# Performance work log

Measured on AMD Instinct MI355X. Metric: run time of the kernel, lower is better.

Reference implementation:

```python
import jax, jax.numpy as jnp
import numpy as np

LAMBDA = 25.0
MU = 25.0
NU = 1.0
ALPHA = 0.25
EPS = 1e-4
NUM_MATCHES = (20, 4)


def _cdist(x, y):
    # x: (B, L1, C), y: (B, L2, C) -> (B, L1, L2) euclidean distances
    x2 = jnp.sum(x * x, axis=-1)[..., :, None]
    y2 = jnp.sum(y * y, axis=-1)[..., None, :]
    d2 = x2 + y2 - 2.0 * jnp.einsum('blc,bmc->blm', x, y)
    return jnp.sqrt(jnp.maximum(d2, 0.0))


def _nearest_neighbors(input_maps, candidate_maps, distances, num_matches):
    # For each input location, its nearest candidate; then keep the
    # num_matches input locations with smallest NN distance, in original order.
    nn_dist = jnp.min(distances, axis=-1)    # (B, L1)
    nn_idx = jnp.argmin(distances, axis=-1)  # (B, L1)
    _, sel = jax.lax.top_k(-nn_dist, num_matches)  # (B, M) smallest distances
    sel = jnp.sort(sel, axis=1)  # restore original ordering of positions
    filtered_input = jnp.take_along_axis(input_maps, sel[..., None], axis=1)
    nn_sel = jnp.take_along_axis(nn_idx, sel, axis=1)
    filtered_candidate = jnp.take_along_axis(candidate_maps, nn_sel[..., None], axis=1)
    return filtered_input, filtered_candidate


def _mse(a, b):
    return jnp.mean((a - b) ** 2)


def _vicreg_loss(z_a, z_b):
    inv_loss = _mse(z_a, z_b)

    def var_loss(z):
        std = jnp.sqrt(jnp.var(z, axis=0, ddof=1) + EPS)
        return jnp.mean(jax.nn.relu(1.0 - std))

    def cov_loss(z):
        n, d = z.shape
        zc = z - jnp.mean(z, axis=0)
        cov = (zc.T @ zc) / (n - 1)
        off = cov - jnp.diag(jnp.diag(cov))
        return jnp.sum(off ** 2) / d

    v = 0.5 * (var_loss(z_a) + var_loss(z_b))
    c = cov_loss(z_a) + cov_loss(z_b)
    return LAMBDA * inv_loss + MU * v + NU * c


def _local_loss(z_global, z_local, grid_global, grid_local):
    B = z_global.shape[0]
    zg = z_global.reshape(B, -1, z_global.shape[-1])   # (B, Lg, C)
    zl = z_local.reshape(B, -1, z_local.shape[-1])     # (B, Ll, C)

    inv_loss = 0.0
    # feature-space NN
    gf, gn = _nearest_neighbors(zg, zl, _cdist(zg, zl), NUM_MATCHES[0])
    lf, ln = _nearest_neighbors(zl, zg, _cdist(zl, zg), NUM_MATCHES[1])
    inv_loss = inv_loss + (_mse(gf, gn) / 2 + _mse(lf, ln) / 2)

    # grid-space NN (distances from grids, gather from feature maps)
    gg = grid_global.reshape(B, -1, 2)
    gl = grid_local.reshape(B, -1, 2)
    gf, gn = _nearest_neighbors(zg, zl, _cdist(gg, gl), NUM_MATCHES[0])
    lf, ln = _nearest_neighbors(zl, zg, _cdist(gl, gg), NUM_MATCHES[1])
    inv_loss = inv_loss + (_mse(gf, gn) / 2 + _mse(lf, ln) / 2)

    return LAMBDA * inv_loss


def setup_inputs() -> dict:
    key = jax.random.key(0)
    ks = jax.random.split(key, 6)
    B, D, C = 32, 8192, 512
    return {
        'z_global': jax.random.normal(ks[0], (B, D), jnp.float32),
        'z_local': jax.random.normal(ks[1], (B, D), jnp.float32),
        'z_global_local_features': jax.random.normal(ks[2], (B, 24, 24, C), jnp.float32),
        'z_local_local_features': jax.random.normal(ks[3], (B, 16, 16, C), jnp.float32),
        'grid_global': jax.random.uniform(ks[4], (B, 24, 24, 2), jnp.float32),
        'grid_local': jax.random.uniform(ks[5], (B, 16, 16, 2), jnp.float32),
    }


def reference(z_global, z_local, z_global_local_features, z_local_local_features, grid_global, grid_local):
    global_loss = _vicreg_loss(z_global, z_local)
    local_loss = _local_loss(z_global_local_features, z_local_local_features, grid_global, grid_local)
    return ALPHA * global_loss + (1.0 - ALPHA) * local_loss
```

## Files before the change

kernel.cpp:

```cpp
#include <hip/hip_runtime.h>
#include <hip/hip_bf16.h>

#define BATCH 32
#define DZ    8192
#define LG    576
#define LL    256
#define CH    512

#define OFF_S      0
#define OFF_BSUM   8192
#define OFF_SELSUM 9472
#define OFF_NG     10496
#define OFF_NL     84224
#define OFF_ROWNN  116992
#define OFF_COLNN  264448
#define OFF_ABF    329984
#define OFF_BBF    19204352
#define WS_NEED    27592960

typedef __attribute__((ext_vector_type(8))) short bf16x8;
typedef __attribute__((ext_vector_type(4))) float f32x4;

__device__ __forceinline__ unsigned short f2bf(float x) {
  union { __hip_bfloat16 h; unsigned short u; } cv;
  cv.h = __float2bfloat16(x);
  return cv.u;
}

__global__ __launch_bounds__(256) void k_front(
    const float* __restrict__ za, const float* __restrict__ zb,
    double* __restrict__ bsum, float* __restrict__ S,
    const float* __restrict__ zgf, const float* __restrict__ zlf,
    unsigned short* __restrict__ Abf, unsigned short* __restrict__ Bbf,
    float* __restrict__ ng, float* __restrict__ nl,
    unsigned long long* __restrict__ nnInit) {
  __shared__ float sred[4][5];
  int tid = threadIdx.x, lane = tid & 63, wv = tid >> 6;
  int blk = blockIdx.x;
  if (blk >= 1088) {
    int row = (blk - 1088) * 4 + wv;
    if (lane == 0) nnInit[row] = ~0ull;
    const float* src; unsigned short* dst; float* nrm;
    if (row < BATCH * LG) {
      src = zgf + (size_t)row * CH; dst = Abf + (size_t)row * CH; nrm = ng + row;
    } else {
      int rr = row - BATCH * LG;
      src = zlf + (size_t)rr * CH; dst = Bbf + (size_t)rr * CH; nrm = nl + rr;
    }
    const float4* s4 = (const float4*)src;
    float4 v0 = s4[lane * 2], v1 = s4[lane * 2 + 1];
    float ss = v0.x * v0.x + v0.y * v0.y + v0.z * v0.z + v0.w * v0.w +
               v1.x * v1.x + v1.y * v1.y + v1.z * v1.z + v1.w * v1.w;
    union { unsigned short h[8]; uint4 u; } pk;
    pk.h[0] = f2bf(v0.x); pk.h[1] = f2bf(v0.y); pk.h[2] = f2bf(v0.z); pk.h[3] = f2bf(v0.w);
    pk.h[4] = f2bf(v1.x); pk.h[5] = f2bf(v1.y); pk.h[6] = f2bf(v1.z); pk.h[7] = f2bf(v1.w);
    *(uint4*)(dst + lane * 8) = pk.u;
    for (int off = 32; off; off >>= 1) ss += __shfl_down(ss, off);
    if (lane == 0) *nrm = ss;
    return;
  }
  if (blk < 32) {
    int i = blk * 256 + tid;
    float sa = 0.f, qa = 0.f, sb = 0.f, qb = 0.f, si = 0.f;
    #pragma unroll 8
    for (int b = 0; b < BATCH; ++b) {
      float va = za[(size_t)b * DZ + i];
      float vb = zb[(size_t)b * DZ + i];
      sa += va; qa += va * va;
      sb += vb; qb += vb * vb;
      float d = va - vb; si += d * d;
    }
    float ssa = qa - sa * sa * (1.f / 32.f);
    float ssb = qb - sb * sb * (1.f / 32.f);
    float v0 = si;
    float v1 = fmaxf(0.f, 1.f - sqrtf(ssa * (1.f / 31.f) + 1e-4f));
    float v2 = fmaxf(0.f, 1.f - sqrtf(ssb * (1.f / 31.f) + 1e-4f));
    float v3 = ssa * ssa, v4 = ssb * ssb;
    for (int off = 32; off; off >>= 1) {
      v0 += __shfl_down(v0, off); v1 += __shfl_down(v1, off);
      v2 += __shfl_down(v2, off); v3 += __shfl_down(v3, off);
      v4 += __shfl_down(v4, off);
    }
    if (lane == 0) {
      sred[wv][0] = v0; sred[wv][1] = v1; sred[wv][2] = v2;
      sred[wv][3] = v3; sred[wv][4] = v4;
    }
    __syncthreads();
    if (tid < 5)
      bsum[blk * 5 + tid] =
          (double)(sred[0][tid] + sred[1][tid] + sred[2][tid] + sred[3][tid]);
  } else {
    int e = blk - 32;
    int zi = e >= 528; if (zi) e -= 528;
    const float* z = zi ? zb : za;
    float* Sz = S + zi * 1024;
    int p = 0, rem = e;
    while (rem >= 32 - p) { rem -= 32 - p; ++p; }
    int q = p + rem;
    const float4* zp = (const float4*)(z + (size_t)p * DZ);
    const float4* zq = (const float4*)(z + (size_t)q * DZ);
    float s = 0.f;
    #pragma unroll
    for (int ii = 0; ii < 8; ++ii) {
      int i = tid + ii * 256;
      float4 a = zp[i], b = zq[i];
      s += a.x * b.x + a.y * b.y + a.z * b.z + a.w * b.w;
    }
    for (int off = 32; off; off >>= 1) s += __shfl_down(s, off);
    if (lane == 0) sred[wv][0] = s;
    __syncthreads();
    if (tid == 0) {
      float r = sred[0][0] + sred[1][0] + sred[2][0] + sred[3][0];
      Sz[p * 32 + q] = r;
      if (p != q) Sz[q * 32 + p] = r;
    }
  }
}

__global__ __launch_bounds__(256) void k_feat_mfma(
    const unsigned short* __restrict__ Abf, const unsigned short* __restrict__ Bbf,
    const float* __restrict__ ng, const float* __restrict__ nl,
    unsigned long long* __restrict__ rowNN, unsigned long long* __restrict__ colNN) {
  const int b = blockIdx.z;
  const int row0 = blockIdx.x * 64;
  const int col0 = blockIdx.y * 128;
  const int tid = threadIdx.x;
  const int wave = tid >> 6, lane = tid & 63;
  const int m16 = lane & 15, quad = lane >> 4;
  const int wm = wave >> 1, wn = wave & 1;

  __shared__ unsigned short As[64][72];
  __shared__ unsigned short Bs[128][72];

  const unsigned short* Ag = Abf + ((size_t)(b * LG + row0)) * CH;
  const unsigned short* Bg = Bbf + ((size_t)(b * LL + col0)) * CH;

  const int sr = tid >> 2, sq = tid & 3;
  const int br = tid >> 1, bq = tid & 1;

  f32x4 acc[2][4] = {};

  for (int k0 = 0; k0 < CH; k0 += 64) {
    uint4 a0 = *(const uint4*)(Ag + (size_t)sr * CH + k0 + sq * 16);
    uint4 a1 = *(const uint4*)(Ag + (size_t)sr * CH + k0 + sq * 16 + 8);
    uint4 b0 = *(const uint4*)(Bg + (size_t)br * CH + k0 + bq * 16);
    uint4 b1 = *(const uint4*)(Bg + (size_t)br * CH + k0 + bq * 16 + 8);
    uint4 b2 = *(const uint4*)(Bg + (size_t)br * CH + k0 + bq * 16 + 32);
    uint4 b3 = *(const uint4*)(Bg + (size_t)br * CH + k0 + bq * 16 + 40);
    __syncthreads();
    *(uint4*)&As[sr][sq * 16] = a0; *(uint4*)&As[sr][sq * 16 + 8] = a1;
    *(uint4*)&Bs[br][bq * 16] = b0; *(uint4*)&Bs[br][bq * 16 + 8] = b1;
    *(uint4*)&Bs[br][bq * 16 + 32] = b2; *(uint4*)&Bs[br][bq * 16 + 40] = b3;
    __syncthreads();
    #pragma unroll
    for (int kk = 0; kk < 64; kk += 32) {
      bf16x8 af0 = *(const bf16x8*)&As[wm * 32 + m16][kk + quad * 8];
      bf16x8 af1 = *(const bf16x8*)&As[wm * 32 + 16 + m16][kk + quad * 8];
      bf16x8 bfv[4];
      #pragma unroll
      for (int j = 0; j < 4; ++j)
        bfv[j] = *(const bf16x8*)&Bs[wn * 64 + j * 16 + m16][kk + quad * 8];
      #pragma unroll
      for (int j = 0; j < 4; ++j) {
        acc[0][j] = __builtin_amdgcn_mfma_f32_16x16x32_bf16(af0, bfv[j], acc[0][j], 0, 0, 0);
        acc[1][j] = __builtin_amdgcn_mfma_f32_16x16x32_bf16(af1, bfv[j], acc[1][j], 0, 0, 0);
      }
    }
  }

  float na[2][4], nb[4];
  #pragma unroll
  for (int i = 0; i < 2; ++i)
    #pragma unroll
    for (int r = 0; r < 4; ++r)
      na[i][r] = ng[b * LG + row0 + wm * 32 + i * 16 + quad * 4 + r];
  #pragma unroll
  for (int j = 0; j < 4; ++j)
    nb[j] = nl[b * LL + col0 + wn * 64 + j * 16 + m16];

  #pragma unroll
  for (int i = 0; i < 2; ++i) {
    #pragma unroll
    for (int r = 0; r < 4; ++r) {
      unsigned long long p = ~0ull;
      #pragma unroll
      for (int j = 0; j < 4; ++j) {
        float d = fmaxf(na[i][r] + nb[j] - 2.f * acc[i][j][r], 0.f);
        unsigned c = (unsigned)(col0 + wn * 64 + j * 16 + m16);
        unsigned long long pj = (((unsigned long long)__float_as_uint(d)) << 32) | c;
        p = pj < p ? pj : p;
      }
      #pragma unroll
      for (int s = 1; s < 16; s <<= 1) {
        unsigned long long q = __shfl_xor(p, s);
        p = q < p ? q : p;
      }
      if (m16 == 0)
        atomicMin(&rowNN[(size_t)b * LG + row0 + wm * 32 + i * 16 + quad * 4 + r], p);
    }
  }
  #pragma unroll
  for (int j = 0; j < 4; ++j) {
    unsigned long long p = ~0ull;
    #pragma unroll
    for (int i = 0; i < 2; ++i) {
      #pragma unroll
      for (int r = 0; r < 4; ++r) {
        float d = fmaxf(na[i][r] + nb[j] - 2.f * acc[i][j][r], 0.f);
        unsigned rg = (unsigned)(row0 + wm * 32 + i * 16 + quad * 4 + r);
        unsigned long long pr = (((unsigned long long)__float_as_uint(d)) << 32) | rg;
        p = pr < p ? pr : p;
      }
    }
    unsigned long long q = __shfl_xor(p, 16); p = q < p ? q : p;
    q = __shfl_xor(p, 32); p = q < p ? q : p;
    if (quad == 0)
      atomicMin(&colNN[(size_t)b * LL + col0 + wn * 64 + j * 16 + m16], p);
  }
}

__global__ __launch_bounds__(64) void k_norms(
    const float* __restrict__ zgf, const float* __restrict__ zlf,
    float* __restrict__ ng, float* __restrict__ nl,
    unsigned long long* __restrict__ nnInit) {
  int r = blockIdx.x;
  if (threadIdx.x == 0) nnInit[r] = ~0ull;
  const float* src; float* dst;
  if (r < BATCH * LG) { src = zgf + (size_t)r * CH; dst = ng + r; }
  else { int rr = r - BATCH * LG; src = zlf + (size_t)rr * CH; dst = nl + rr; }
  float s = 0.f;
  for (int j = threadIdx.x; j < CH; j += 64) { float v = src[j]; s += v * v; }
  for (int off = 32; off > 0; off >>= 1) s += __shfl_down(s, off);
  if (threadIdx.x == 0) *dst = s;
}

__global__ __launch_bounds__(256) void k_feat_nn(
    const float* __restrict__ zgf, const float* __restrict__ zlf,
    const float* __restrict__ ng, const float* __restrict__ nl,
    unsigned long long* __restrict__ rowNN, unsigned long long* __restrict__ colNN) {
  const int b = blockIdx.z;
  const int row0 = blockIdx.x * 64;
  const int col0 = blockIdx.y * 128;
  const int tid = threadIdx.x;
  const int tx = tid & 15, ty = tid >> 4;
  __shared__ float As[64][20];
  __shared__ float Bs[128][20];
  __shared__ float Ds[64][130];
  const float* Ag = zgf + ((size_t)b * LG + row0) * CH;
  const float* Bg = zlf + ((size_t)b * LL + col0) * CH;
  float acc[4][8];
  #pragma unroll
  for (int i = 0; i < 4; ++i)
    #pragma unroll
    for (int j = 0; j < 8; ++j) acc[i][j] = 0.f;
  const int ar = tid >> 2;
  const int ak = (tid & 3) * 4;
  for (int k0 = 0; k0 < CH; k0 += 16) {
    float4 av  = *(const float4*)(Ag + (size_t)ar * CH + k0 + ak);
    float4 bv0 = *(const float4*)(Bg + (size_t)ar * CH + k0 + ak);
    float4 bv1 = *(const float4*)(Bg + (size_t)(ar + 64) * CH + k0 + ak);
    __syncthreads();
    *(float4*)&As[ar][ak] = av;
    *(float4*)&Bs[ar][ak] = bv0;
    *(float4*)&Bs[ar + 64][ak] = bv1;
    __syncthreads();
    #pragma unroll
    for (int k = 0; k < 16; ++k) {
      float a0 = As[ty][k], a1 = As[ty + 16][k], a2 = As[ty + 32][k], a3 = As[ty + 48][k];
      float bv[8];
      #pragma unroll
      for (int j = 0; j < 8; ++j) bv[j] = Bs[tx + 16 * j][k];
      #pragma unroll
      for (int j = 0; j < 8; ++j) {
        acc[0][j] += a0 * bv[j]; acc[1][j] += a1 * bv[j];
        acc[2][j] += a2 * bv[j]; acc[3][j] += a3 * bv[j];
      }
    }
  }
  float ngr[4], nlc[8];
  #pragma unroll
  for (int i = 0; i < 4; ++i) ngr[i] = ng[b * LG + row0 + ty + 16 * i];
  #pragma unroll
  for (int j = 0; j < 8; ++j) nlc[j] = nl[b * LL + col0 + tx + 16 * j];
  #pragma unroll
  for (int i = 0; i < 4; ++i)
    #pragma unroll
    for (int j = 0; j < 8; ++j)
      Ds[ty + 16 * i][tx + 16 * j] = fmaxf(ngr[i] + nlc[j] - 2.f * acc[i][j], 0.f);
  __syncthreads();
  if (tid < 64) {
    unsigned long long best = ~0ull;
    for (int c = 0; c < 128; ++c) {
      unsigned long long p =
          ((unsigned long long)__float_as_uint(Ds[tid][c]) << 32) | (unsigned)(col0 + c);
      best = p < best ? p : best;
    }
    atomicMin(&rowNN[(size_t)b * LG + row0 + tid], best);
  } else if (tid < 192) {
    int c = tid - 64;
    unsigned long long best = ~0ull;
    for (int r = 0; r < 64; ++r) {
      unsigned long long p =
          ((unsigned long long)__float_as_uint(Ds[r][c]) << 32) | (unsigned)(row0 + r);
      best = p < best ? p : best;
    }
    atomicMin(&colNN[(size_t)b * LL + col0 + c], best);
  }
}

struct SelSmem {
  unsigned long long keys[LG];
  unsigned int nnm[LG];
  float cxy[2 * LG];
  unsigned int plist[40];
  unsigned int cnt;
  float fred[4];
};

template <int V>
__device__ __forceinline__ void sel_case(
    SelSmem& sm, int b,
    const float* __restrict__ zgf, const float* __restrict__ zlf,
    const float* __restrict__ gg, const float* __restrict__ gl,
    const unsigned long long* __restrict__ rowNN,
    const unsigned long long* __restrict__ colNN,
    double* __restrict__ selsum) {
  constexpr bool GDIR = (V == 0 || V == 2);
  constexpr int L1 = GDIR ? LG : LL;
  constexpr int L2 = GDIR ? LL : LG;
  constexpr int M  = GDIR ? 20 : 4;
  constexpr int NR = (L1 + 255) / 256;
  const float* fin  = GDIR ? zgf + (size_t)b * LG * CH : zlf + (size_t)b * LL * CH;
  const float* fcan = GDIR ? zlf + (size_t)b * LL * CH : zgf + (size_t)b * LG * CH;
  int tid = threadIdx.x, lane = tid & 63, wv = tid >> 6;
  if (tid == 0) sm.cnt = 0;

  if constexpr (V < 2) {
    const unsigned long long* src =
        (V == 0) ? rowNN + (size_t)b * LG : colNN + (size_t)b * LL;
    #pragma unroll
    for (int s = 0; s < NR; ++s) {
      int l = tid + s * 256;
      if (l < L1) {
        unsigned long long p = src[l];
        sm.keys[l] = (p & 0xFFFFFFFF00000000ull) | (unsigned)l;
        sm.nnm[l] = (unsigned)(p & 0xFFFFFFFFu);
      }
    }
  } else {
    const float* gin  = (V == 2) ? gg + (size_t)b * LG * 2 : gl + (size_t)b * LL * 2;
    const float* gcan = (V == 2) ? gl + (size_t)b * LL * 2 : gg + (size_t)b * LG * 2;
    #pragma unroll
    for (int s = 0; s < (2 * L2 + 255) / 256; ++s) {
      int i = tid + s * 256;
      if (i < 2 * L2) sm.cxy[i] = gcan[i];
    }
    __syncthreads();
    float x[NR], y[NR], bd[NR];
    unsigned bi[NR];
    #pragma unroll
    for (int s = 0; s < NR; ++s) {
      int l = tid + s * 256;
      x[s] = (l < L1) ? gin[2 * l] : 0.f;
      y[s] = (l < L1) ? gin[2 * l + 1] : 0.f;
      bd[s] = 3.4e38f; bi[s] = 0;
    }
    const float2* c2 = (const float2*)sm.cxy;
    for (int m2 = 0; m2 < L2; m2 += 8) {
      float2 cc[8];
      #pragma unroll
      for (int u = 0; u < 8; ++u) cc[u] = c2[m2 + u];
      #pragma unroll
      for (int u = 0; u < 8; ++u)
        #pragma unroll
        for (int s = 0; s < NR; ++s) {
          float dx = x[s] - cc[u].x, dy = y[s] - cc[u].y;
          float d2 = dx * dx + dy * dy;
          if (d2 < bd[s]) { bd[s] = d2; bi[s] = (unsigned)(m2 + u); }
        }
    }
    #pragma unroll
    for (int s = 0; s < NR; ++s) {
      int l = tid + s * 256;
      if (l < L1) {
        sm.keys[l] = ((unsigned long long)__float_as_uint(bd[s]) << 32) | (unsigned)l;
        sm.nnm[l] = bi[s];
      }
    }
  }
  __syncthreads();

  unsigned long long myk[NR];
  int rk[NR];
  #pragma unroll
  for (int s = 0; s < NR; ++s) {
    int l = tid + s * 256;
    myk[s] = (l < L1) ? sm.keys[l] : ~0ull;
    rk[s] = 0;
  }
  for (int j = 0; j < L1; j += 8) {
    unsigned long long kk[8];
    #pragma unroll
    for (int u = 0; u < 8; ++u) kk[u] = sm.keys[j + u];
    #pragma unroll
    for (int u = 0; u < 8; ++u)
      #pragma unroll
      for (int s = 0; s < NR; ++s) rk[s] += (kk[u] < myk[s]) ? 1 : 0;
  }
  #pragma unroll
  for (int s = 0; s < NR; ++s) {
    int l = tid + s * 256;
    if (l < L1 && rk[s] < M) {
      unsigned slot = atomicAdd(&sm.cnt, 1u);
      sm.plist[2 * slot] = (unsigned)l;
      sm.plist[2 * slot + 1] = sm.nnm[l];
    }
  }
  __syncthreads();

  float part = 0.f;
  #pragma unroll
  for (int rr = 0; rr < M / 4; ++rr) {
    int r = wv + rr * 4;
    const float4* a4 = (const float4*)(fin + (size_t)sm.plist[2 * r] * CH);
    const float4* c4 = (const float4*)(fcan + (size_t)sm.plist[2 * r + 1] * CH);
    float4 xa = a4[lane * 2], xb = a4[lane * 2 + 1];
    float4 ya = c4[lane * 2], yb = c4[lane * 2 + 1];
    float d0 = xa.x - ya.x, d1 = xa.y - ya.y, d2 = xa.z - ya.z, d3 = xa.w - ya.w;
    float d4 = xb.x - yb.x, d5 = xb.y - yb.y, d6 = xb.z - yb.z, d7 = xb.w - yb.w;
    part += d0 * d0 + d1 * d1 + d2 * d2 + d3 * d3 +
            d4 * d4 + d5 * d5 + d6 * d6 + d7 * d7;
  }
  for (int s = 32; s; s >>= 1) part += __shfl_down(part, s);
  if (lane == 0) sm.fred[wv] = part;
  __syncthreads();
  if (tid == 0)
    selsum[V * 32 + b] = (double)(sm.fred[0] + sm.fred[1] + sm.fred[2] + sm.fred[3]);
}

__global__ __launch_bounds__(256) void k_sel(
    const float* __restrict__ zgf, const float* __restrict__ zlf,
    const float* __restrict__ gg, const float* __restrict__ gl,
    const unsigned long long* __restrict__ rowNN,
    const unsigned long long* __restrict__ colNN,
    double* __restrict__ selsum) {
  __shared__ SelSmem sm;
  int b = blockIdx.x;
  switch (blockIdx.y) {
    case 0: sel_case<0>(sm, b, zgf, zlf, gg, gl, rowNN, colNN, selsum); break;
    case 1: sel_case<1>(sm, b, zgf, zlf, gg, gl, rowNN, colNN, selsum); break;
    case 2: sel_case<2>(sm, b, zgf, zlf, gg, gl, rowNN, colNN, selsum); break;
    default: sel_case<3>(sm, b, zgf, zlf, gg, gl, rowNN, colNN, selsum); break;
  }
}

__global__ __launch_bounds__(64) void k_final(
    const double* __restrict__ bsum, const double* __restrict__ selsum,
    const float* __restrict__ S, float* __restrict__ out) {
  __shared__ float t[2][32];
  __shared__ double sacc[5];
  __shared__ double smf[4];
  int lane = threadIdx.x;
  #pragma unroll
  for (int zi = 0; zi < 2; ++zi) {
    if (lane < 32) {
      float tp = 0.f;
      for (int bb = 0; bb < 32; ++bb) tp += S[zi * 1024 + lane * 32 + bb];
      t[zi][lane] = tp * (1.f / 32.f);
    }
  }
  if (lane < 5) {
    double s = 0.0;
    for (int blk = 0; blk < 32; ++blk) s += bsum[blk * 5 + lane];
    sacc[lane] = s;
  }
  if (lane >= 8 && lane < 12) {
    int v = lane - 8;
    double s = 0.0;
    for (int bb = 0; bb < 32; ++bb) s += selsum[v * 32 + bb];
    smf[v] = s;
  }
  __syncthreads();
  double total[2];
  #pragma unroll
  for (int zi = 0; zi < 2; ++zi) {
    float u = 0.f;
    for (int bb = 0; bb < 32; ++bb) u += t[zi][bb];
    u *= (1.f / 32.f);
    double s = 0.0;
    for (int e = lane; e < 1024; e += 64) {
      int p = e >> 5, q = e & 31;
      float G = S[zi * 1024 + e] - t[zi][p] - t[zi][q] + u;
      s += (double)G * (double)G;
    }
    for (int off = 32; off; off >>= 1) s += __shfl_down(s, off);
    total[zi] = s;
  }
  if (lane == 0) {
    double inv_g = sacc[0] / (32.0 * 8192.0);
    double v = 0.5 * (sacc[1] + sacc[2]) / 8192.0;
    double c = (total[0] - sacc[3] + total[1] - sacc[4]) / (961.0 * 8192.0);
    double gloss = 25.0 * inv_g + 25.0 * v + c;
    double mfg = smf[0] / (32.0 * 20.0 * 512.0);
    double mfl = smf[1] / (32.0 * 4.0 * 512.0);
    double mgg = smf[2] / (32.0 * 20.0 * 512.0);
    double mgl = smf[3] / (32.0 * 4.0 * 512.0);
    double lloss = 25.0 * (0.5 * (mfg + mfl) + 0.5 * (mgg + mgl));
    out[0] = (float)(0.25 * gloss + 0.75 * lloss);
  }
}

extern "C" void kernel_launch(void* const* d_in, const int* in_sizes, int n_in,
                              void* d_out, int out_size, void* d_ws, size_t ws_size,
                              hipStream_t stream) {
  const float* zg  = (const float*)d_in[0];
  const float* zl  = (const float*)d_in[1];
  const float* zgf = (const float*)d_in[2];
  const float* zlf = (const float*)d_in[3];
  const float* gg  = (const float*)d_in[4];
  const float* glo = (const float*)d_in[5];

  char* ws = (char*)d_ws;
  float* S       = (float*)(ws + OFF_S);
  double* bsum   = (double*)(ws + OFF_BSUM);
  double* selsum = (double*)(ws + OFF_SELSUM);
  float* ng = (float*)(ws + OFF_NG);
  float* nl = (float*)(ws + OFF_NL);
  unsigned long long* rowNN = (unsigned long long*)(ws + OFF_ROWNN);
  unsigned long long* colNN = (unsigned long long*)(ws + OFF_COLNN);
  unsigned short* Abf = (unsigned short*)(ws + OFF_ABF);
  unsigned short* Bbf = (unsigned short*)(ws + OFF_BBF);

  if (ws_size >= WS_NEED) {
    k_front<<<32 + 1056 + (BATCH * (LG + LL)) / 4, 256, 0, stream>>>(
        zg, zl, bsum, S, zgf, zlf, Abf, Bbf, ng, nl, rowNN);
    k_feat_mfma<<<dim3(LG / 64, LL / 128, BATCH), 256, 0, stream>>>(
        Abf, Bbf, ng, nl, rowNN, colNN);
  } else {
    k_front<<<32 + 1056, 256, 0, stream>>>(
        zg, zl, bsum, S, zgf, zlf, Abf, Bbf, ng, nl, rowNN);
    k_norms<<<BATCH * (LG + LL), 64, 0, stream>>>(zgf, zlf, ng, nl, rowNN);
    k_feat_nn<<<dim3(LG / 64, LL / 128, BATCH), 256, 0, stream>>>(zgf, zlf, ng, nl, rowNN, colNN);
  }
  k_sel<<<dim3(BATCH, 4), 256, 0, stream>>>(zgf, zlf, gg, glo, rowNN, colNN, selsum);
  k_final<<<1, 64, 0, stream>>>(bsum, selsum, S, (float*)d_out);
}
```

Before: 162.0 us.

## Fuse bf16 conversion and norms into MFMA kernel; merge launches into mega and tail kernels

The features are now converted fp32→bf16 inside the MFMA tile loader, and squared norms are accumulated during the same loads. This removes the separate bf16 workspace pass and its extra global round trip. Nearest-neighbour results are written as per-tile partials and reduced at selection time, which replaces atomicMin and the init pass. The global VICReg work and the grid-space selection cases run in the same launch as the distance GEMM. The final reduction moves into the last tail block via a done counter, cutting launches from four to two. In exchange, the fp32 tiles are reloaded and converted redundantly across column tiles, and tail selection has to read more partial entries.

```diff
diff --git a/kernel.cpp b/kernel.cpp
--- a/kernel.cpp
+++ b/kernel.cpp
@@ -10,13 +10,10 @@
 #define OFF_S      0
 #define OFF_BSUM   8192
 #define OFF_SELSUM 9472
-#define OFF_NG     10496
-#define OFF_NL     84224
-#define OFF_ROWNN  116992
-#define OFF_COLNN  264448
-#define OFF_ABF    329984
-#define OFF_BBF    19204352
-#define WS_NEED    27592960
+#define OFF_DONE   10496
+#define OFF_RNP    10560
+#define OFF_CNP    305472
+#define WS_NEED    895296
 
 typedef __attribute__((ext_vector_type(8))) short bf16x8;
 typedef __attribute__((ext_vector_type(4))) float f32x4;
@@ -27,285 +24,15 @@
   return cv.u;
 }
 
-__global__ __launch_bounds__(256) void k_front(
-    const float* __restrict__ za, const float* __restrict__ zb,
-    double* __restrict__ bsum, float* __restrict__ S,
-    const float* __restrict__ zgf, const float* __restrict__ zlf,
-    unsigned short* __restrict__ Abf, unsigned short* __restrict__ Bbf,
-    float* __restrict__ ng, float* __restrict__ nl,
-    unsigned long long* __restrict__ nnInit) {
-  __shared__ float sred[4][5];
-  int tid = threadIdx.x, lane = tid & 63, wv = tid >> 6;
-  int blk = blockIdx.x;
-  if (blk >= 1088) {
-    int row = (blk - 1088) * 4 + wv;
-    if (lane == 0) nnInit[row] = ~0ull;
-    const float* src; unsigned short* dst; float* nrm;
-    if (row < BATCH * LG) {
-      src = zgf + (size_t)row * CH; dst = Abf + (size_t)row * CH; nrm = ng + row;
-    } else {
-      int rr = row - BATCH * LG;
-      src = zlf + (size_t)rr * CH; dst = Bbf + (size_t)rr * CH; nrm = nl + rr;
-    }
-    const float4* s4 = (const float4*)src;
-    float4 v0 = s4[lane * 2], v1 = s4[lane * 2 + 1];
-    float ss = v0.x * v0.x + v0.y * v0.y + v0.z * v0.z + v0.w * v0.w +
-               v1.x * v1.x + v1.y * v1.y + v1.z * v1.z + v1.w * v1.w;
-    union { unsigned short h[8]; uint4 u; } pk;
-    pk.h[0] = f2bf(v0.x); pk.h[1] = f2bf(v0.y); pk.h[2] = f2bf(v0.z); pk.h[3] = f2bf(v0.w);
-    pk.h[4] = f2bf(v1.x); pk.h[5] = f2bf(v1.y); pk.h[6] = f2bf(v1.z); pk.h[7] = f2bf(v1.w);
-    *(uint4*)(dst + lane * 8) = pk.u;
-    for (int off = 32; off; off >>= 1) ss += __shfl_down(ss, off);
-    if (lane == 0) *nrm = ss;
-    return;
-  }
-  if (blk < 32) {
-    int i = blk * 256 + tid;
-    float sa = 0.f, qa = 0.f, sb = 0.f, qb = 0.f, si = 0.f;
-    #pragma unroll 8
-    for (int b = 0; b < BATCH; ++b) {
-      float va = za[(size_t)b * DZ + i];
-      float vb = zb[(size_t)b * DZ + i];
-      sa += va; qa += va * va;
-      sb += vb; qb += vb * vb;
-      float d = va - vb; si += d * d;
-    }
-    float ssa = qa - sa * sa * (1.f / 32.f);
-    float ssb = qb - sb * sb * (1.f / 32.f);
-    float v0 = si;
-    float v1 = fmaxf(0.f, 1.f - sqrtf(ssa * (1.f / 31.f) + 1e-4f));
-    float v2 = fmaxf(0.f, 1.f - sqrtf(ssb * (1.f / 31.f) + 1e-4f));
-    float v3 = ssa * ssa, v4 = ssb * ssb;
-    for (int off = 32; off; off >>= 1) {
-      v0 += __shfl_down(v0, off); v1 += __shfl_down(v1, off);
-      v2 += __shfl_down(v2, off); v3 += __shfl_down(v3, off);
-      v4 += __shfl_down(v4, off);
-    }
-    if (lane == 0) {
-      sred[wv][0] = v0; sred[wv][1] = v1; sred[wv][2] = v2;
-      sred[wv][3] = v3; sred[wv][4] = v4;
-    }
-    __syncthreads();
-    if (tid < 5)
-      bsum[blk * 5 + tid] =
-          (double)(sred[0][tid] + sred[1][tid] + sred[2][tid] + sred[3][tid]);
-  } else {
-    int e = blk - 32;
-    int zi = e >= 528; if (zi) e -= 528;
-    const float* z = zi ? zb : za;
-    float* Sz = S + zi * 1024;
-    int p = 0, rem = e;
-    while (rem >= 32 - p) { rem -= 32 - p; ++p; }
-    int q = p + rem;
-    const float4* zp = (const float4*)(z + (size_t)p * DZ);
-    const float4* zq = (const float4*)(z + (size_t)q * DZ);
-    float s = 0.f;
-    #pragma unroll
-    for (int ii = 0; ii < 8; ++ii) {
-      int i = tid + ii * 256;
-      float4 a = zp[i], b = zq[i];
-      s += a.x * b.x + a.y * b.y + a.z * b.z + a.w * b.w;
-    }
-    for (int off = 32; off; off >>= 1) s += __shfl_down(s, off);
-    if (lane == 0) sred[wv][0] = s;
-    __syncthreads();
-    if (tid == 0) {
-      float r = sred[0][0] + sred[1][0] + sred[2][0] + sred[3][0];
-      Sz[p * 32 + q] = r;
-      if (p != q) Sz[q * 32 + p] = r;
-    }
-  }
-}
-
-__global__ __launch_bounds__(256) void k_feat_mfma(
-    const unsigned short* __restrict__ Abf, const unsigned short* __restrict__ Bbf,
-    const float* __restrict__ ng, const float* __restrict__ nl,
-    unsigned long long* __restrict__ rowNN, unsigned long long* __restrict__ colNN) {
-  const int b = blockIdx.z;
-  const int row0 = blockIdx.x * 64;
-  const int col0 = blockIdx.y * 128;
-  const int tid = threadIdx.x;
-  const int wave = tid >> 6, lane = tid & 63;
-  const int m16 = lane & 15, quad = lane >> 4;
-  const int wm = wave >> 1, wn = wave & 1;
-
-  __shared__ unsigned short As[64][72];
-  __shared__ unsigned short Bs[128][72];
-
-  const unsigned short* Ag = Abf + ((size_t)(b * LG + row0)) * CH;
-  const unsigned short* Bg = Bbf + ((size_t)(b * LL + col0)) * CH;
-
-  const int sr = tid >> 2, sq = tid & 3;
-  const int br = tid >> 1, bq = tid & 1;
-
-  f32x4 acc[2][4] = {};
-
-  for (int k0 = 0; k0 < CH; k0 += 64) {
-    uint4 a0 = *(const uint4*)(Ag + (size_t)sr * CH + k0 + sq * 16);
-    uint4 a1 = *(const uint4*)(Ag + (size_t)sr * CH + k0 + sq * 16 + 8);
-    uint4 b0 = *(const uint4*)(Bg + (size_t)br * CH + k0 + bq * 16);
-    uint4 b1 = *(const uint4*)(Bg + (size_t)br * CH + k0 + bq * 16 + 8);
-    uint4 b2 = *(const uint4*)(Bg + (size_t)br * CH + k0 + bq * 16 + 32);
-    uint4 b3 = *(const uint4*)(Bg + (size_t)br * CH + k0 + bq * 16 + 40);
-    __syncthreads();
-    *(uint4*)&As[sr][sq * 16] = a0; *(uint4*)&As[sr][sq * 16 + 8] = a1;
-    *(uint4*)&Bs[br][bq * 16] = b0; *(uint4*)&Bs[br][bq * 16 + 8] = b1;
-    *(uint4*)&Bs[br][bq * 16 + 32] = b2; *(uint4*)&Bs[br][bq * 16 + 40] = b3;
-    __syncthreads();
-    #pragma unroll
-    for (int kk = 0; kk < 64; kk += 32) {
-      bf16x8 af0 = *(const bf16x8*)&As[wm * 32 + m16][kk + quad * 8];
-      bf16x8 af1 = *(const bf16x8*)&As[wm * 32 + 16 + m16][kk + quad * 8];
-      bf16x8 bfv[4];
-      #pragma unroll
-      for (int j = 0; j < 4; ++j)
-        bfv[j] = *(const bf16x8*)&Bs[wn * 64 + j * 16 + m16][kk + quad * 8];
-      #pragma unroll
-      for (int j = 0; j < 4; ++j) {
-        acc[0][j] = __builtin_amdgcn_mfma_f32_16x16x32_bf16(af0, bfv[j], acc[0][j], 0, 0, 0);
-        acc[1][j] = __builtin_amdgcn_mfma_f32_16x16x32_bf16(af1, bfv[j], acc[1][j], 0, 0, 0);
-      }
-    }
-  }
-
-  float na[2][4], nb[4];
-  #pragma unroll
-  for (int i = 0; i < 2; ++i)
-    #pragma unroll
-    for (int r = 0; r < 4; ++r)
-      na[i][r] = ng[b * LG + row0 + wm * 32 + i * 16 + quad * 4 + r];
-  #pragma unroll
-  for (int j = 0; j < 4; ++j)
-    nb[j] = nl[b * LL + col0 + wn * 64 + j * 16 + m16];
-
-  #pragma unroll
-  for (int i = 0; i < 2; ++i) {
-    #pragma unroll
-    for (int r = 0; r < 4; ++r) {
-      unsigned long long p = ~0ull;
-      #pragma unroll
-      for (int j = 0; j < 4; ++j) {
-        float d = fmaxf(na[i][r] + nb[j] - 2.f * acc[i][j][r], 0.f);
-        unsigned c = (unsigned)(col0 + wn * 64 + j * 16 + m16);
-        unsigned long long pj = (((unsigned long long)__float_as_uint(d)) << 32) | c;
-        p = pj < p ? pj : p;
-      }
-      #pragma unroll
-      for (int s = 1; s < 16; s <<= 1) {
-        unsigned long long q = __shfl_xor(p, s);
-        p = q < p ? q : p;
-      }
-      if (m16 == 0)
-        atomicMin(&rowNN[(size_t)b * LG + row0 + wm * 32 + i * 16 + quad * 4 + r], p);
-    }
-  }
-  #pragma unroll
-  for (int j = 0; j < 4; ++j) {
-    unsigned long long p = ~0ull;
-    #pragma unroll
-    for (int i = 0; i < 2; ++i) {
-      #pragma unroll
-      for (int r = 0; r < 4; ++r) {
-        float d = fmaxf(na[i][r] + nb[j] - 2.f * acc[i][j][r], 0.f);
-        unsigned rg = (unsigned)(row0 + wm * 32 + i * 16 + quad * 4 + r);
-        unsigned long long pr = (((unsigned long long)__float_as_uint(d)) << 32) | rg;
-        p = pr < p ? pr : p;
-      }
-    }
-    unsigned long long q = __shfl_xor(p, 16); p = q < p ? q : p;
-    q = __shfl_xor(p, 32); p = q < p ? q : p;
-    if (quad == 0)
-      atomicMin(&colNN[(size_t)b * LL + col0 + wn * 64 + j * 16 + m16], p);
-  }
-}
-
-__global__ __launch_bounds__(64) void k_norms(
-    const float* __restrict__ zgf, const float* __restrict__ zlf,
-    float* __restrict__ ng, float* __restrict__ nl,
-    unsigned long long* __restrict__ nnInit) {
-  int r = blockIdx.x;
-  if (threadIdx.x == 0) nnInit[r] = ~0ull;
-  const float* src; float* dst;
-  if (r < BATCH * LG) { src = zgf + (size_t)r * CH; dst = ng + r; }
-  else { int rr = r - BATCH * LG; src = zlf + (size_t)rr * CH; dst = nl + rr; }
-  float s = 0.f;
-  for (int j = threadIdx.x; j < CH; j += 64) { float v = src[j]; s += v * v; }
-  for (int off = 32; off > 0; off >>= 1) s += __shfl_down(s, off);
-  if (threadIdx.x == 0) *dst = s;
-}
-
-__global__ __launch_bounds__(256) void k_feat_nn(
-    const float* __restrict__ zgf, const float* __restrict__ zlf,
-    const float* __restrict__ ng, const float* __restrict__ nl,
-    unsigned long long* __restrict__ rowNN, unsigned long long* __restrict__ colNN) {
-  const int b = blockIdx.z;
-  const int row0 = blockIdx.x * 64;
-  const int col0 = blockIdx.y * 128;
-  const int tid = threadIdx.x;
-  const int tx = tid & 15, ty = tid >> 4;
-  __shared__ float As[64][20];
-  __shared__ float Bs[128][20];
-  __shared__ float Ds[64][130];
-  const float* Ag = zgf + ((size_t)b * LG + row0) * CH;
-  const float* Bg = zlf + ((size_t)b * LL + col0) * CH;
-  float acc[4][8];
-  #pragma unroll
-  for (int i = 0; i < 4; ++i)
-    #pragma unroll
-    for (int j = 0; j < 8; ++j) acc[i][j] = 0.f;
-  const int ar = tid >> 2;
-  const int ak = (tid & 3) * 4;
-  for (int k0 = 0; k0 < CH; k0 += 16) {
-    float4 av  = *(const float4*)(Ag + (size_t)ar * CH + k0 + ak);
-    float4 bv0 = *(const float4*)(Bg + (size_t)ar * CH + k0 + ak);
-    float4 bv1 = *(const float4*)(Bg + (size_t)(ar + 64) * CH + k0 + ak);
-    __syncthreads();
-    *(float4*)&As[ar][ak] = av;
-    *(float4*)&Bs[ar][ak] = bv0;
-    *(float4*)&Bs[ar + 64][ak] = bv1;
-    __syncthreads();
-    #pragma unroll
-    for (int k = 0; k < 16; ++k) {
-      float a0 = As[ty][k], a1 = As[ty + 16][k], a2 = As[ty + 32][k], a3 = As[ty + 48][k];
-      float bv[8];
-      #pragma unroll
-      for (int j = 0; j < 8; ++j) bv[j] = Bs[tx + 16 * j][k];
-      #pragma unroll
-      for (int j = 0; j < 8; ++j) {
-        acc[0][j] += a0 * bv[j]; acc[1][j] += a1 * bv[j];
-        acc[2][j] += a2 * bv[j]; acc[3][j] += a3 * bv[j];
-      }
-    }
-  }
-  float ngr[4], nlc[8];
-  #pragma unroll
-  for (int i = 0; i < 4; ++i) ngr[i] = ng[b * LG + row0 + ty + 16 * i];
-  #pragma unroll
-  for (int j = 0; j < 8; ++j) nlc[j] = nl[b * LL + col0 + tx + 16 * j];
-  #pragma unroll
-  for (int i = 0; i < 4; ++i)
-    #pragma unroll
-    for (int j = 0; j < 8; ++j)
-      Ds[ty + 16 * i][tx + 16 * j] = fmaxf(ngr[i] + nlc[j] - 2.f * acc[i][j], 0.f);
-  __syncthreads();
-  if (tid < 64) {
-    unsigned long long best = ~0ull;
-    for (int c = 0; c < 128; ++c) {
-      unsigned long long p =
-          ((unsigned long long)__float_as_uint(Ds[tid][c]) << 32) | (unsigned)(col0 + c);
-      best = p < best ? p : best;
-    }
-    atomicMin(&rowNN[(size_t)b * LG + row0 + tid], best);
-  } else if (tid < 192) {
-    int c = tid - 64;
-    unsigned long long best = ~0ull;
-    for (int r = 0; r < 64; ++r) {
-      unsigned long long p =
-          ((unsigned long long)__float_as_uint(Ds[r][c]) << 32) | (unsigned)(row0 + r);
-      best = p < best ? p : best;
-    }
-    atomicMin(&colNN[(size_t)b * LL + col0 + c], best);
-  }
+__device__ __forceinline__ uint4 pack8(float4 lo, float4 hi) {
+  union { unsigned short h[8]; uint4 u; } pk;
+  pk.h[0] = f2bf(lo.x); pk.h[1] = f2bf(lo.y); pk.h[2] = f2bf(lo.z); pk.h[3] = f2bf(lo.w);
+  pk.h[4] = f2bf(hi.x); pk.h[5] = f2bf(hi.y); pk.h[6] = f2bf(hi.z); pk.h[7] = f2bf(hi.w);
+  return pk.u;
+}
+
+__device__ __forceinline__ float dot4(float4 v) {
+  return v.x * v.x + v.y * v.y + v.z * v.z + v.w * v.w;
 }
 
 struct SelSmem {
@@ -322,8 +49,8 @@
     SelSmem& sm, int b,
     const float* __restrict__ zgf, const float* __restrict__ zlf,
     const float* __restrict__ gg, const float* __restrict__ gl,
-    const unsigned long long* __restrict__ rowNN,
-    const unsigned long long* __restrict__ colNN,
+    const unsigned long long* __restrict__ rowNNp,
+    const unsigned long long* __restrict__ colNNp,
     double* __restrict__ selsum) {
   constexpr bool GDIR = (V == 0 || V == 2);
   constexpr int L1 = GDIR ? LG : LL;
@@ -336,13 +63,17 @@
   if (tid == 0) sm.cnt = 0;
 
   if constexpr (V < 2) {
+    constexpr int P = (V == 0) ? 2 : 9;
     const unsigned long long* src =
-        (V == 0) ? rowNN + (size_t)b * LG : colNN + (size_t)b * LL;
+        (V == 0) ? rowNNp + (size_t)b * LG * 2 : colNNp + (size_t)b * LL * 9;
     #pragma unroll
     for (int s = 0; s < NR; ++s) {
       int l = tid + s * 256;
       if (l < L1) {
-        unsigned long long p = src[l];
+        const unsigned long long* q = src + (size_t)l * P;
+        unsigned long long p = q[0];
+        #pragma unroll
+        for (int u = 1; u < P; ++u) { unsigned long long t2 = q[u]; p = t2 < p ? t2 : p; }
         sm.keys[l] = (p & 0xFFFFFFFF00000000ull) | (unsigned)l;
         sm.nnm[l] = (unsigned)(p & 0xFFFFFFFFu);
       }
@@ -438,75 +169,291 @@
     selsum[V * 32 + b] = (double)(sm.fred[0] + sm.fred[1] + sm.fred[2] + sm.fred[3]);
 }
 
-__global__ __launch_bounds__(256) void k_sel(
+__global__ __launch_bounds__(256) void k_mega(
+    const float* __restrict__ za, const float* __restrict__ zb,
     const float* __restrict__ zgf, const float* __restrict__ zlf,
     const float* __restrict__ gg, const float* __restrict__ gl,
-    const unsigned long long* __restrict__ rowNN,
-    const unsigned long long* __restrict__ colNN,
-    double* __restrict__ selsum) {
-  __shared__ SelSmem sm;
-  int b = blockIdx.x;
-  switch (blockIdx.y) {
-    case 0: sel_case<0>(sm, b, zgf, zlf, gg, gl, rowNN, colNN, selsum); break;
-    case 1: sel_case<1>(sm, b, zgf, zlf, gg, gl, rowNN, colNN, selsum); break;
-    case 2: sel_case<2>(sm, b, zgf, zlf, gg, gl, rowNN, colNN, selsum); break;
-    default: sel_case<3>(sm, b, zgf, zlf, gg, gl, rowNN, colNN, selsum); break;
-  }
-}
-
-__global__ __launch_bounds__(64) void k_final(
-    const double* __restrict__ bsum, const double* __restrict__ selsum,
-    const float* __restrict__ S, float* __restrict__ out) {
-  __shared__ float t[2][32];
-  __shared__ double sacc[5];
-  __shared__ double smf[4];
-  int lane = threadIdx.x;
-  #pragma unroll
-  for (int zi = 0; zi < 2; ++zi) {
-    if (lane < 32) {
+    double* __restrict__ bsum, float* __restrict__ S,
+    unsigned long long* __restrict__ rowNNp, unsigned long long* __restrict__ colNNp,
+    double* __restrict__ selsum, unsigned int* __restrict__ doneCnt) {
+  __shared__ __align__(16) char smem[28416];
+  int tid = threadIdx.x, lane = tid & 63, wv = tid >> 6;
+  int blk = blockIdx.x;
+
+  if (blk < 576) {
+    int fs = (blk & 7) * 72 + (blk >> 3);
+    int b = fs / 18, rr_ = fs % 18;
+    int by = rr_ / 9, bx = rr_ % 9;
+    int row0 = bx * 64, col0 = by * 128;
+
+    unsigned short (*As)[72] = (unsigned short(*)[72])smem;
+    unsigned short (*Bs)[72] = (unsigned short(*)[72])(smem + 9216);
+    float* Asn = (float*)(smem + 27648);
+    float* Bsn = (float*)(smem + 27904);
+
+    const int m16 = lane & 15, quad = lane >> 4;
+    const int wm = wv >> 1, wn = wv & 1;
+    const float* Ag = zgf + ((size_t)(b * LG + row0)) * CH;
+    const float* Bg = zlf + ((size_t)(b * LL + col0)) * CH;
+    const int sr = tid >> 2, sq = tid & 3;
+    const int br = tid >> 1, bq = tid & 1;
+
+    f32x4 acc[2][4] = {};
+    float ssA = 0.f, ssB = 0.f;
+
+    for (int k0 = 0; k0 < CH; k0 += 64) {
+      const float* ap = Ag + (size_t)sr * CH + k0 + sq * 16;
+      float4 a0 = *(const float4*)(ap);
+      float4 a1 = *(const float4*)(ap + 4);
+      float4 a2 = *(const float4*)(ap + 8);
+      float4 a3 = *(const float4*)(ap + 12);
+      const float* bp = Bg + (size_t)br * CH + k0 + bq * 16;
+      float4 b0 = *(const float4*)(bp);
+      float4 b1 = *(const float4*)(bp + 4);
+      float4 b2 = *(const float4*)(bp + 8);
+      float4 b3 = *(const float4*)(bp + 12);
+      float4 b4 = *(const float4*)(bp + 32);
+      float4 b5 = *(const float4*)(bp + 36);
+      float4 b6 = *(const float4*)(bp + 40);
+      float4 b7 = *(const float4*)(bp + 44);
+      ssA += dot4(a0) + dot4(a1) + dot4(a2) + dot4(a3);
+      ssB += dot4(b0) + dot4(b1) + dot4(b2) + dot4(b3) +
+             dot4(b4) + dot4(b5) + dot4(b6) + dot4(b7);
+      __syncthreads();
+      *(uint4*)&As[sr][sq * 16]      = pack8(a0, a1);
+      *(uint4*)&As[sr][sq * 16 + 8]  = pack8(a2, a3);
+      *(uint4*)&Bs[br][bq * 16]      = pack8(b0, b1);
+      *(uint4*)&Bs[br][bq * 16 + 8]  = pack8(b2, b3);
+      *(uint4*)&Bs[br][bq * 16 + 32] = pack8(b4, b5);
+      *(uint4*)&Bs[br][bq * 16 + 40] = pack8(b6, b7);
+      __syncthreads();
+      #pragma unroll
+      for (int kk = 0; kk < 64; kk += 32) {
+        bf16x8 af0 = *(const bf16x8*)&As[wm * 32 + m16][kk + quad * 8];
+        bf16x8 af1 = *(const bf16x8*)&As[wm * 32 + 16 + m16][kk + quad * 8];
+        bf16x8 bfv[4];
+        #pragma unroll
+        for (int j = 0; j < 4; ++j)
+          bfv[j] = *(const bf16x8*)&Bs[wn * 64 + j * 16 + m16][kk + quad * 8];
+        #pragma unroll
+        for (int j = 0; j < 4; ++j) {
+          acc[0][j] = __builtin_amdgcn_mfma_f32_16x16x32_bf16(af0, bfv[j], acc[0][j], 0, 0, 0);
+          acc[1][j] = __builtin_amdgcn_mfma_f32_16x16x32_bf16(af1, bfv[j], acc[1][j], 0, 0, 0);
+        }
+      }
+    }
+
+    ssA += __shfl_xor(ssA, 1); ssA += __shfl_xor(ssA, 2);
+    ssB += __shfl_xor(ssB, 1);
+    if (sq == 0) Asn[sr] = ssA;
+    if (bq == 0) Bsn[br] = ssB;
+    __syncthreads();
+
+    float na[2][4], nb[4];
+    #pragma unroll
+    for (int i = 0; i < 2; ++i)
+      #pragma unroll
+      for (int r = 0; r < 4; ++r)
+        na[i][r] = Asn[wm * 32 + i * 16 + quad * 4 + r];
+    #pragma unroll
+    for (int j = 0; j < 4; ++j)
+      nb[j] = Bsn[wn * 64 + j * 16 + m16];
+
+    #pragma unroll
+    for (int i = 0; i < 2; ++i) {
+      #pragma unroll
+      for (int r = 0; r < 4; ++r) {
+        unsigned long long p = ~0ull;
+        #pragma unroll
+        for (int j = 0; j < 4; ++j) {
+          float d = fmaxf(na[i][r] + nb[j] - 2.f * acc[i][j][r], 0.f);
+          unsigned c = (unsigned)(col0 + wn * 64 + j * 16 + m16);
+          unsigned long long pj = (((unsigned long long)__float_as_uint(d)) << 32) | c;
+          p = pj < p ? pj : p;
+        }
+        #pragma unroll
+        for (int s = 1; s < 16; s <<= 1) {
+          unsigned long long q = __shfl_xor(p, s);
+          p = q < p ? q : p;
+        }
+        if (m16 == 0)
+          rowNNp[((size_t)b * LG + row0 + wm * 32 + i * 16 + quad * 4 + r) * 2 + by] = p;
+      }
+    }
+    #pragma unroll
+    for (int j = 0; j < 4; ++j) {
+      unsigned long long p = ~0ull;
+      #pragma unroll
+      for (int i = 0; i < 2; ++i) {
+        #pragma unroll
+        for (int r = 0; r < 4; ++r) {
+          float d = fmaxf(na[i][r] + nb[j] - 2.f * acc[i][j][r], 0.f);
+          unsigned rg = (unsigned)(row0 + wm * 32 + i * 16 + quad * 4 + r);
+          unsigned long long pr = (((unsigned long long)__float_as_uint(d)) << 32) | rg;
+          p = pr < p ? pr : p;
+        }
+      }
+      unsigned long long q = __shfl_xor(p, 16); p = q < p ? q : p;
+      q = __shfl_xor(p, 32); p = q < p ? q : p;
+      if (quad == 0)
+        colNNp[((size_t)b * LL + col0 + wn * 64 + j * 16 + m16) * 9 + bx] = p;
+    }
+    return;
+  }
+
+  if (blk < 608) {
+    float (*sred)[5] = (float(*)[5])smem;
+    int blkS = blk - 576;
+    if (blkS == 0 && tid == 0) *doneCnt = 0;
+    int i = blkS * 256 + tid;
+    float sa = 0.f, qa = 0.f, sb = 0.f, qb = 0.f, si = 0.f;
+    #pragma unroll 8
+    for (int b = 0; b < BATCH; ++b) {
+      float va = za[(size_t)b * DZ + i];
+      float vb = zb[(size_t)b * DZ + i];
+      sa += va; qa += va * va;
+      sb += vb; qb += vb * vb;
+      float d = va - vb; si += d * d;
+    }
+    float ssa = qa - sa * sa * (1.f / 32.f);
+    float ssb = qb - sb * sb * (1.f / 32.f);
+    float v0 = si;
+    float v1 = fmaxf(0.f, 1.f - sqrtf(ssa * (1.f / 31.f) + 1e-4f));
+    float v2 = fmaxf(0.f, 1.f - sqrtf(ssb * (1.f / 31.f) + 1e-4f));
+    float v3 = ssa * ssa, v4 = ssb * ssb;
+    for (int off = 32; off; off >>= 1) {
+      v0 += __shfl_down(v0, off); v1 += __shfl_down(v1, off);
+      v2 += __shfl_down(v2, off); v3 += __shfl_down(v3, off);
+      v4 += __shfl_down(v4, off);
+    }
+    if (lane == 0) {
+      sred[wv][0] = v0; sred[wv][1] = v1; sred[wv][2] = v2;
+      sred[wv][3] = v3; sred[wv][4] = v4;
+    }
+    __syncthreads();
+    if (tid < 5)
+      bsum[blkS * 5 + tid] =
+          (double)(sred[0][tid] + sred[1][tid] + sred[2][tid] + sred[3][tid]);
+    return;
+  }
+
+  if (blk < 1664) {
+    float (*sred)[5] = (float(*)[5])smem;
+    int e = blk - 608;
+    int zi = e >= 528; if (zi) e -= 528;
+    const float* z = zi ? zb : za;
+    float* Sz = S + zi * 1024;
+    int p = 0, rem = e;
+    while (rem >= 32 - p) { rem -= 32 - p; ++p; }
+    int q = p + rem;
+    const float4* zp = (const float4*)(z + (size_t)p * DZ);
+    const float4* zq = (const float4*)(z + (size_t)q * DZ);
+    float s = 0.f;
+    #pragma unroll
+    for (int ii = 0; ii < 8; ++ii) {
+      int i = tid + ii * 256;
+      float4 a = zp[i], bb = zq[i];
+      s += a.x * bb.x + a.y * bb.y + a.z * bb.z + a.w * bb.w;
+    }
+    for (int off = 32; off; off >>= 1) s += __shfl_down(s, off);
+    if (lane == 0) sred[wv][0] = s;
+    __syncthreads();
+    if (tid == 0) {
+      float r = sred[0][0] + sred[1][0] + sred[2][0] + sred[3][0];
+      Sz[p * 32 + q] = r;
+      if (p != q) Sz[q * 32 + p] = r;
+    }
+    return;
+  }
+
+  {
+    SelSmem& sm = *reinterpret_cast<SelSmem*>(smem);
+    int e = blk - 1664;
+    int b2 = e >> 1;
+    if (e & 1) sel_case<3>(sm, b2, zgf, zlf, gg, gl, rowNNp, colNNp, selsum);
+    else       sel_case<2>(sm, b2, zgf, zlf, gg, gl, rowNNp, colNNp, selsum);
+  }
+}
+
+struct TailSmem {
+  SelSmem sel;
+  float t[2][32];
+  double sacc[5];
+  double smf[4];
+  int isLast;
+};
+
+__global__ __launch_bounds__(256) void k_tail(
+    const float* __restrict__ zgf, const float* __restrict__ zlf,
+    const float* __restrict__ gg, const float* __restrict__ gl,
+    const unsigned long long* __restrict__ rowNNp,
+    const unsigned long long* __restrict__ colNNp,
+    double* __restrict__ selsum, const double* __restrict__ bsum,
+    const float* __restrict__ S, unsigned int* __restrict__ doneCnt,
+    float* __restrict__ out) {
+  __shared__ TailSmem ts;
+  int tid = threadIdx.x;
+  int b = blockIdx.x >> 1, V = blockIdx.x & 1;
+  if (V == 0) sel_case<0>(ts.sel, b, zgf, zlf, gg, gl, rowNNp, colNNp, selsum);
+  else        sel_case<1>(ts.sel, b, zgf, zlf, gg, gl, rowNNp, colNNp, selsum);
+
+  if (tid == 0) {
+    __threadfence();
+    unsigned r = atomicAdd(doneCnt, 1u);
+    ts.isLast = (r == 63) ? 1 : 0;
+  }
+  __syncthreads();
+  if (!ts.isLast) return;
+  __threadfence();
+
+  if (tid < 32) {
+    #pragma unroll
+    for (int zi = 0; zi < 2; ++zi) {
       float tp = 0.f;
-      for (int bb = 0; bb < 32; ++bb) tp += S[zi * 1024 + lane * 32 + bb];
-      t[zi][lane] = tp * (1.f / 32.f);
-    }
-  }
-  if (lane < 5) {
+      for (int bb = 0; bb < 32; ++bb) tp += S[zi * 1024 + tid * 32 + bb];
+      ts.t[zi][tid] = tp * (1.f / 32.f);
+    }
+  }
+  if (tid < 5) {
     double s = 0.0;
-    for (int blk = 0; blk < 32; ++blk) s += bsum[blk * 5 + lane];
-    sacc[lane] = s;
-  }
-  if (lane >= 8 && lane < 12) {
-    int v = lane - 8;
+    for (int blk = 0; blk < 32; ++blk) s += bsum[blk * 5 + tid];
+    ts.sacc[tid] = s;
+  }
+  if (tid >= 8 && tid < 12) {
+    int v = tid - 8;
     double s = 0.0;
     for (int bb = 0; bb < 32; ++bb) s += selsum[v * 32 + bb];
-    smf[v] = s;
+    ts.smf[v] = s;
   }
   __syncthreads();
-  double total[2];
-  #pragma unroll
-  for (int zi = 0; zi < 2; ++zi) {
-    float u = 0.f;
-    for (int bb = 0; bb < 32; ++bb) u += t[zi][bb];
-    u *= (1.f / 32.f);
-    double s = 0.0;
-    for (int e = lane; e < 1024; e += 64) {
-      int p = e >> 5, q = e & 31;
-      float G = S[zi * 1024 + e] - t[zi][p] - t[zi][q] + u;
-      s += (double)G * (double)G;
-    }
-    for (int off = 32; off; off >>= 1) s += __shfl_down(s, off);
-    total[zi] = s;
-  }
-  if (lane == 0) {
-    double inv_g = sacc[0] / (32.0 * 8192.0);
-    double v = 0.5 * (sacc[1] + sacc[2]) / 8192.0;
-    double c = (total[0] - sacc[3] + total[1] - sacc[4]) / (961.0 * 8192.0);
-    double gloss = 25.0 * inv_g + 25.0 * v + c;
-    double mfg = smf[0] / (32.0 * 20.0 * 512.0);
-    double mfl = smf[1] / (32.0 * 4.0 * 512.0);
-    double mgg = smf[2] / (32.0 * 20.0 * 512.0);
-    double mgl = smf[3] / (32.0 * 4.0 * 512.0);
-    double lloss = 25.0 * (0.5 * (mfg + mfl) + 0.5 * (mgg + mgl));
-    out[0] = (float)(0.25 * gloss + 0.75 * lloss);
+  if (tid < 64) {
+    double total[2];
+    #pragma unroll
+    for (int zi = 0; zi < 2; ++zi) {
+      float u = 0.f;
+      for (int bb = 0; bb < 32; ++bb) u += ts.t[zi][bb];
+      u *= (1.f / 32.f);
+      double s = 0.0;
+      for (int e = tid; e < 1024; e += 64) {
+        int p = e >> 5, q = e & 31;
+        float G = S[zi * 1024 + e] - ts.t[zi][p] - ts.t[zi][q] + u;
+        s += (double)G * (double)G;
+      }
+      for (int off = 32; off; off >>= 1) s += __shfl_down(s, off);
+      total[zi] = s;
+    }
+    if (tid == 0) {
+      double inv_g = ts.sacc[0] / (32.0 * 8192.0);
+      double v = 0.5 * (ts.sacc[1] + ts.sacc[2]) / 8192.0;
+      double c = (total[0] - ts.sacc[3] + total[1] - ts.sacc[4]) / (961.0 * 8192.0);
+      double gloss = 25.0 * inv_g + 25.0 * v + c;
+      double mfg = ts.smf[0] / (32.0 * 20.0 * 512.0);
+      double mfl = ts.smf[1] / (32.0 * 4.0 * 512.0);
+      double mgg = ts.smf[2] / (32.0 * 20.0 * 512.0);
+      double mgl = ts.smf[3] / (32.0 * 4.0 * 512.0);
+      double lloss = 25.0 * (0.5 * (mfg + mfl) + 0.5 * (mgg + mgl));
+      out[0] = (float)(0.25 * gloss + 0.75 * lloss);
+    }
   }
 }
 
@@ -524,24 +471,12 @@
   float* S       = (float*)(ws + OFF_S);
   double* bsum   = (double*)(ws + OFF_BSUM);
   double* selsum = (double*)(ws + OFF_SELSUM);
-  float* ng = (float*)(ws + OFF_NG);
-  float* nl = (float*)(ws + OFF_NL);
-  unsigned long long* rowNN = (unsigned long long*)(ws + OFF_ROWNN);
-  unsigned long long* colNN = (unsigned long long*)(ws + OFF_COLNN);
-  unsigned short* Abf = (unsigned short*)(ws + OFF_ABF);
-  unsigned short* Bbf = (unsigned short*)(ws + OFF_BBF);
-
-  if (ws_size >= WS_NEED) {
-    k_front<<<32 + 1056 + (BATCH * (LG + LL)) / 4, 256, 0, stream>>>(
-        zg, zl, bsum, S, zgf, zlf, Abf, Bbf, ng, nl, rowNN);
-    k_feat_mfma<<<dim3(LG / 64, LL / 128, BATCH), 256, 0, stream>>>(
-        Abf, Bbf, ng, nl, rowNN, colNN);
-  } else {
-    k_front<<<32 + 1056, 256, 0, stream>>>(
-        zg, zl, bsum, S, zgf, zlf, Abf, Bbf, ng, nl, rowNN);
-    k_norms<<<BATCH * (LG + LL), 64, 0, stream>>>(zgf, zlf, ng, nl, rowNN);
-    k_feat_nn<<<dim3(LG / 64, LL / 128, BATCH), 256, 0, stream>>>(zgf, zlf, ng, nl, rowNN, colNN);
-  }
-  k_sel<<<dim3(BATCH, 4), 256, 0, stream>>>(zgf, zlf, gg, glo, rowNN, colNN, selsum);
-  k_final<<<1, 64, 0, stream>>>(bsum, selsum, S, (float*)d_out);
-}
+  unsigned int* doneCnt = (unsigned int*)(ws + OFF_DONE);
+  unsigned long long* rowNNp = (unsigned long long*)(ws + OFF_RNP);
+  unsigned long long* colNNp = (unsigned long long*)(ws + OFF_CNP);
+
+  k_mega<<<1728, 256, 0, stream>>>(zg, zl, zgf, zlf, gg, glo,
+                                   bsum, S, rowNNp, colNNp, selsum, doneCnt);
+  k_tail<<<64, 256, 0, stream>>>(zgf, zlf, gg, glo, rowNNp, colNNp,
+                                 selsum, bsum, S, doneCnt, (float*)d_out);
+}
```

New measurement: 159.4 us. About the same (-1.6%).
